# Optimization experiments

Measured on AMD Instinct MI355X. Metric: run time of the kernel, lower is better.

## Reference

```python
import jax, jax.numpy as jnp
import numpy as np


def _conv2d(x, w, b):
    # 3x3, stride 1, pad 1, NCHW
    y = jax.lax.conv_general_dilated(x, w, (1, 1), [(1, 1), (1, 1)],
                                     dimension_numbers=('NCHW', 'OIHW', 'NCHW'))
    return y + b[None, :, None, None]


def _bilinear(img, py, px):
    # img: [B,C,H,W]; py/px: [B,H,W] float sample coords; zero padding outside
    B, C, H, W = img.shape
    y0f = jnp.floor(py)
    x0f = jnp.floor(px)
    wy = (py - y0f)[:, None]  # [B,1,H,W]
    wx = (px - x0f)[:, None]
    y0 = y0f.astype(jnp.int32)
    x0 = x0f.astype(jnp.int32)
    flat = img.reshape(B, C, H * W)

    def g(iy, ix):
        valid = (iy >= 0) & (iy < H) & (ix >= 0) & (ix < W)
        idx = (jnp.clip(iy, 0, H - 1) * W + jnp.clip(ix, 0, W - 1)).reshape(B, 1, H * W)
        v = jnp.take_along_axis(flat, idx, axis=2).reshape(B, C, H, W)
        return v * valid[:, None].astype(img.dtype)

    return (g(y0, x0) * (1 - wy) * (1 - wx)
            + g(y0, x0 + 1) * (1 - wy) * wx
            + g(y0 + 1, x0) * wy * (1 - wx)
            + g(y0 + 1, x0 + 1) * wy * wx)


def _deform_conv(x, offset, w, b):
    # torchvision DeformConv2d v1: kernel 3, stride 1, pad 1, dil 1, no mask
    # offset: [B, 18, H, W]; channels (2k, 2k+1) = (dy, dx) for kernel tap k (row-major)
    B, C, H, W = x.shape
    gy = jnp.arange(H, dtype=x.dtype)[:, None]   # [H,1]
    gx = jnp.arange(W, dtype=x.dtype)[None, :]   # [1,W]
    acc = jnp.zeros((B, w.shape[0], H, W), x.dtype)
    for k in range(9):  # small fixed kernel loop keeps intermediates O(B*C*H*W)
        ky, kx = k // 3, k % 3
        py = gy + (ky - 1) + offset[:, 2 * k]
        px = gx + (kx - 1) + offset[:, 2 * k + 1]
        samp = _bilinear(x, py, px)                      # [B,C,H,W]
        acc = acc + jnp.einsum('bchw,oc->bohw', samp, w[:, :, ky, kx])
    return acc + b[None, :, None, None]


def setup_inputs() -> dict:
    key = jax.random.key(0)
    ks = jax.random.split(key, 4)
    B, C, H, W = 4, 64, 256, 256
    return {
        'content_feats': jax.random.normal(ks[0], (B, C, H, W), jnp.float32),
        'blur_feats': jax.random.normal(ks[1], (B, C, H, W), jnp.float32),
        'offset_w': jax.random.normal(ks[2], (27, C, 3, 3), jnp.float32) * 0.02,
        'offset_b': jnp.zeros((27,), jnp.float32),
        'dc_w': jax.random.normal(ks[3], (C, C, 3, 3), jnp.float32) * 0.05,
        'dc_b': jnp.zeros((C,), jnp.float32),
    }


def reference(content_feats, blur_feats, offset_w, offset_b, dc_w, dc_b):
    ow = _conv2d(blur_feats, offset_w, offset_b)   # [B,27,H,W]
    offset = ow[:, :18]                            # first 2*3*3 channels are offsets
    out = _deform_conv(content_feats, offset, dc_w, dc_b)
    return (out, offset)
```

## Files before the change

kernel.cpp:

```cpp
#include <hip/hip_runtime.h>

#define BB 4
#define CC 64
#define HH 256
#define WW 256
#define HWHW 65536

typedef __bf16 bf16x8 __attribute__((ext_vector_type(8)));
typedef float f32x16 __attribute__((ext_vector_type(16)));
typedef unsigned int uint2v __attribute__((ext_vector_type(2)));

__device__ __forceinline__ unsigned short f32_to_bf16(float s) {
    unsigned int xi = __builtin_bit_cast(unsigned int, s);
    unsigned int r = (xi + 0x7fffu + ((xi >> 16) & 1u)) >> 16;
    return (unsigned short)r;
}

__global__ void prep_weights(const float* __restrict__ offset_w,
                             const float* __restrict__ dc_w,
                             float* __restrict__ wA,
                             unsigned short* __restrict__ WB2) {
    int idx = blockIdx.x * 256 + threadIdx.x;
    const int NA = CC * 9 * 18;
    const int NB = 4 * 18 * 64 * 8;
    if (idx < NA) {
        int c = idx / (9 * 18);
        int k = (idx / 18) % 9;
        int o = idx % 18;
        wA[idx] = offset_w[(o * CC + c) * 9 + k];
    }
    int j = idx - NA;
    if (j >= 0 && j < NB) {
        int chunk = j / 9216;
        int rem = j - chunk * 9216;
        int kslot = rem >> 9;
        int n = (rem >> 3) & 63;
        int jj = rem & 7;
        int k_local = kslot * 8 + jj;
        int tap = k_local >> 4;
        int c_local = k_local & 15;
        int c = chunk * 16 + c_local;
        WB2[j] = f32_to_bf16(dc_w[(n * CC + c) * 9 + tap]);
    }
}

__global__ __launch_bounds__(256) void offset_conv(
    const float* __restrict__ blur, const float* __restrict__ wA,
    const float* __restrict__ ob, float* __restrict__ offout) {
    const int x = threadIdx.x;
    const int y = blockIdx.x & (HH - 1);
    const int b = blockIdx.x >> 8;

    int rb[3], cx[3];
    float m[9];
#pragma unroll
    for (int dy = 0; dy < 3; ++dy) {
        int yy = y + dy - 1;
        rb[dy] = min(max(yy, 0), HH - 1) * WW;
        bool vy = (yy >= 0) && (yy < HH);
#pragma unroll
        for (int dx = 0; dx < 3; ++dx) {
            int xx = x + dx - 1;
            bool v = vy && (xx >= 0) && (xx < WW);
            m[dy * 3 + dx] = v ? 1.0f : 0.0f;
        }
    }
#pragma unroll
    for (int dx = 0; dx < 3; ++dx) cx[dx] = min(max(x + dx - 1, 0), WW - 1);

    float acc[18];
#pragma unroll
    for (int o = 0; o < 18; ++o) acc[o] = ob[o];

    const float* img = blur + (size_t)b * CC * HWHW;
    for (int c = 0; c < CC; ++c) {
        const float* pl = img + c * HWHW;
        float s[9];
#pragma unroll
        for (int dy = 0; dy < 3; ++dy)
#pragma unroll
            for (int dx = 0; dx < 3; ++dx)
                s[dy * 3 + dx] = pl[rb[dy] + cx[dx]] * m[dy * 3 + dx];

        const float* wp = wA + c * 9 * 18;
#pragma unroll
        for (int k = 0; k < 9; ++k) {
            float sv = s[k];
#pragma unroll
            for (int o = 0; o < 18; ++o)
                acc[o] = fmaf(sv, wp[k * 18 + o], acc[o]);
        }
    }

    float* op = offout + ((size_t)b * 18) * HWHW + y * WW + x;
#pragma unroll
    for (int o = 0; o < 18; ++o) op[(size_t)o * HWHW] = acc[o];
}

__global__ __launch_bounds__(256) void nchw_to_nhwc(
    const float* __restrict__ in, float* __restrict__ ct) {
    __shared__ float tile[64][65];
    const int t = threadIdx.x;
    const int blk = blockIdx.x;
    const int xseg = blk & 3;
    const int y = (blk >> 2) & (HH - 1);
    const int b = blk >> 10;
    const int px = t & 63;
    const int q = t >> 6;

    const float* src = in + (size_t)b * CC * HWHW + y * WW + xseg * 64;
#pragma unroll
    for (int i = 0; i < 16; ++i) {
        const int c = i * 4 + q;
        tile[c][px] = src[(size_t)c * HWHW + px];
    }
    __syncthreads();
    float* dst = ct + ((size_t)b * HWHW + y * WW + xseg * 64) * 64;
#pragma unroll
    for (int i = 0; i < 16; ++i) {
        const int p = i * 4 + q;
        dst[(size_t)p * 64 + px] = tile[px][p];
    }
}

__global__ __launch_bounds__(256, 4) void deform_mfma_nhwc(
    const float* __restrict__ ct, const float* __restrict__ offs,
    const unsigned short* __restrict__ WB2, const float* __restrict__ bias,
    float* __restrict__ out) {
    __shared__ __align__(16) char ldsbuf[36864];
    unsigned int* sampU = (unsigned int*)ldsbuf;
    float4* stateW = (float4*)(ldsbuf + 18432);
    uint4* stateV = (uint4*)(ldsbuf + 27648);
    float* ldsOut = (float*)ldsbuf;

    const int t = threadIdx.x;
    const int blk = blockIdx.x;
    const int xseg = blk & 3;
    const int y = (blk >> 2) & (HH - 1);
    const int b = blk >> 10;

    {
        const float* offbase = offs + (size_t)b * 18 * HWHW + y * WW + xseg * 64;
        for (int i = t; i < 576; i += 256) {
            const int p = i & 63;
            const int tap = i >> 6;
            const int ky = tap / 3, kx = tap - ky * 3;
            const float offy = offbase[(size_t)(2 * tap) * HWHW + p];
            const float offx = offbase[(size_t)(2 * tap + 1) * HWHW + p];
            const float py = (float)(y + ky - 1) + offy;
            const float pxf = (float)(xseg * 64 + p + kx - 1) + offx;
            const float y0f = floorf(py), x0f = floorf(pxf);
            const float wy = py - y0f, wx = pxf - x0f;
            const int y0 = (int)y0f, x0 = (int)x0f;

            float a00 = (1.0f - wy) * (1.0f - wx);
            float a01 = (1.0f - wy) * wx;
            float a10 = wy * (1.0f - wx);
            float a11 = wy * wx;
            const bool vy0 = (y0 >= 0) && (y0 < HH);
            const bool vy1 = (y0 + 1 >= 0) && (y0 + 1 < HH);
            const bool vx0 = (x0 >= 0) && (x0 < WW);
            const bool vx1 = (x0 + 1 >= 0) && (x0 + 1 < WW);
            float4 w;
            w.x = (vy0 && vx0) ? a00 : 0.0f;
            w.y = (vy0 && vx1) ? a01 : 0.0f;
            w.z = (vy1 && vx0) ? a10 : 0.0f;
            w.w = (vy1 && vx1) ? a11 : 0.0f;

            const int y0c = min(max(y0, 0), HH - 1);
            const int y1c = min(max(y0 + 1, 0), HH - 1);
            const int x0c = min(max(x0, 0), WW - 1);
            const int x1c = min(max(x0 + 1, 0), WW - 1);
            const unsigned int v00 = (unsigned int)(y0c * WW + x0c) << 8;
            const unsigned int dxb = (unsigned int)(x1c - x0c) << 8;
            const unsigned int dyb = (unsigned int)(y1c - y0c) << 16;

            stateW[i] = w;
            uint4 v;
            v.x = v00;
            v.y = v00 + dxb;
            v.z = v00 + dyb;
            v.w = v00 + dyb + dxb;
            stateV[i] = v;
        }
    }
    __syncthreads();

    const char* ctb = (const char*)(ct + (size_t)b * HWHW * 64);

    f32x16 acc = {0, 0, 0, 0, 0, 0, 0, 0, 0, 0, 0, 0, 0, 0, 0, 0};

    const int lane = t & 63;
    const int wv = t >> 6;
    const int l3 = lane >> 3;
    const int clb = (lane & 7) * 8;
    const int hlf = lane >> 5;
    const int l31 = lane & 31;
    const int px_i = ((wv >> 1) * 32) + l31;
    const int n_i = ((wv & 1) * 32) + l31;

    for (int chunk = 0; chunk < 4; ++chunk) {
        {
            const int cb = chunk * 64 + clb;
#pragma unroll 6
            for (int it = 0; it < 18; ++it) {
                const int j = wv * 144 + it * 8 + l3;
                const float4 w = stateW[j];
                const uint4 vo = stateV[j];
                const float2 v00 = *(const float2*)(ctb + (vo.x + cb));
                const float2 v01 = *(const float2*)(ctb + (vo.y + cb));
                const float2 v10 = *(const float2*)(ctb + (vo.z + cb));
                const float2 v11 = *(const float2*)(ctb + (vo.w + cb));
                const float s0 = w.x * v00.x + w.y * v01.x + w.z * v10.x + w.w * v11.x;
                const float s1 = w.x * v00.y + w.y * v01.y + w.z * v10.y + w.w * v11.y;
                unsigned int pk;
                asm("v_cvt_pk_bf16_f32 %0, %1, %2" : "=v"(pk) : "v"(s0), "v"(s1));
                const int tap = j >> 6;
                const int px = j & 63;
                sampU[(tap * 2 + ((lane >> 2) & 1)) * 256 + px * 4 + (lane & 3)] = pk;
            }
        }
        __syncthreads();

        {
            const bf16x8* sampV = (const bf16x8*)sampU;
            const bf16x8* wV = (const bf16x8*)(WB2 + (size_t)chunk * 9216);
#pragma unroll
            for (int ks = 0; ks < 9; ++ks) {
                bf16x8 fa = sampV[(ks * 2 + hlf) * 64 + px_i];
                bf16x8 fb = wV[(ks * 2 + hlf) * 64 + n_i];
                acc = __builtin_amdgcn_mfma_f32_32x32x16_bf16(fa, fb, acc, 0, 0, 0);
            }
        }
        __syncthreads();
    }

    {
        const int n_l = (wv & 1) * 32 + l31;
        const int px_base = (wv >> 1) * 32 + 4 * hlf;
#pragma unroll
        for (int r = 0; r < 16; ++r) {
            const int row = px_base + (r & 3) + 8 * (r >> 2);
            ldsOut[n_l * 65 + row] = acc[r];
        }
    }
    __syncthreads();
    {
        float* base = out + (size_t)b * CC * HWHW + y * WW + xseg * 64;
        for (int i = t; i < 4096; i += 256) {
            const int n = i >> 6;
            const int p = i & 63;
            base[(size_t)n * HWHW + p] = ldsOut[n * 65 + p] + bias[n];
        }
    }
}

__global__ __launch_bounds__(256) void deform_mfma_gather(
    const float* __restrict__ content, const float* __restrict__ offs,
    const unsigned short* __restrict__ WB2, const float* __restrict__ bias,
    float* __restrict__ out) {
    __shared__ __align__(16) char ldsbuf[29952];
    unsigned int* sampU = (unsigned int*)ldsbuf;
    float4* stateW = (float4*)(ldsbuf + 18432);
    unsigned int* stateI = (unsigned int*)(ldsbuf + 27648);
    float* ldsOut = (float*)ldsbuf;

    const int t = threadIdx.x;
    const int px = t & 63;
    const int cg = t >> 6;
    const int blk = blockIdx.x;
    const int xseg = blk & 3;
    const int y = (blk >> 2) & (HH - 1);
    const int b = blk >> 10;

    {
        const float* offbase = offs + (size_t)b * 18 * HWHW + y * WW + xseg * 64;
        for (int i = t; i < 576; i += 256) {
            const int p = i & 63;
            const int tap = i >> 6;
            const int ky = tap / 3, kx = tap - ky * 3;
            const float offy = offbase[(size_t)(2 * tap) * HWHW + p];
            const float offx = offbase[(size_t)(2 * tap + 1) * HWHW + p];
            const float py = (float)(y + ky - 1) + offy;
            const float pxf = (float)(xseg * 64 + p + kx - 1) + offx;
            const float y0f = floorf(py), x0f = floorf(pxf);
            const float wy = py - y0f, wx = pxf - x0f;
            const int y0 = (int)y0f, x0 = (int)x0f;
            float a00 = (1.0f - wy) * (1.0f - wx);
            float a01 = (1.0f - wy) * wx;
            float a10 = wy * (1.0f - wx);
            float a11 = wy * wx;
            const bool vy0 = (y0 >= 0) && (y0 < HH);
            const bool vy1 = (y0 + 1 >= 0) && (y0 + 1 < HH);
            const bool vx0 = (x0 >= 0) && (x0 < WW);
            const bool vx1 = (x0 + 1 >= 0) && (x0 + 1 < WW);
            float4 w;
            w.x = (vy0 && vx0) ? a00 : 0.0f;
            w.y = (vy0 && vx1) ? a01 : 0.0f;
            w.z = (vy1 && vx0) ? a10 : 0.0f;
            w.w = (vy1 && vx1) ? a11 : 0.0f;
            const int y0c = min(max(y0, 0), HH - 1);
            const int y1c = min(max(y0 + 1, 0), HH - 1);
            const int x0c = min(max(x0, 0), WW - 1);
            const int x1c = min(max(x0 + 1, 0), WW - 1);
            stateW[i] = w;
            stateI[i] = (unsigned int)(y0c * WW + x0c) |
                        ((unsigned int)(x1c - x0c) << 16) |
                        ((unsigned int)(y1c - y0c) << 17);
        }
    }
    __syncthreads();

    const float* img = content + (size_t)b * CC * HWHW;
    f32x16 acc = {0, 0, 0, 0, 0, 0, 0, 0, 0, 0, 0, 0, 0, 0, 0, 0};
    const int lane = t & 63;
    const int hlf = lane >> 5;
    const int l31 = lane & 31;
    const int px_i = ((cg >> 1) * 32) + l31;
    const int n_i = ((cg & 1) * 32) + l31;

    for (int chunk = 0; chunk < 4; ++chunk) {
        const int cbase = (chunk * 16 + cg * 4) << 16;
#pragma unroll 3
        for (int tap = 0; tap < 9; ++tap) {
            const float4 w = stateW[tap * 64 + px];
            const unsigned int ii = stateI[tap * 64 + px];
            const int i0 = (int)(ii & 0xFFFFu);
            const int dx = (int)((ii >> 16) & 1u);
            const int dyw = ((int)((ii >> 17) & 1u)) << 8;
            unsigned int pk0 = 0, pk1 = 0;
#pragma unroll
            for (int i = 0; i < 4; ++i) {
                const int cb = cbase + (i << 16);
                const float v00 = img[cb + i0];
                const float v01 = img[cb + i0 + dx];
                const float v10 = img[cb + i0 + dyw];
                const float v11 = img[cb + i0 + dyw + dx];
                const float s = w.x * v00 + w.y * v01 + w.z * v10 + w.w * v11;
                const unsigned int u = f32_to_bf16(s);
                if (i == 0) pk0 = u;
                else if (i == 1) pk0 |= u << 16;
                else if (i == 2) pk1 = u;
                else pk1 |= u << 16;
            }
            uint2v v2 = {pk0, pk1};
            *(uint2v*)&sampU[(tap * 2 + (cg >> 1)) * 256 + px * 4 + (cg & 1) * 2] = v2;
        }
        __syncthreads();
        {
            const bf16x8* sampV = (const bf16x8*)sampU;
            const bf16x8* wV = (const bf16x8*)(WB2 + (size_t)chunk * 9216);
#pragma unroll
            for (int ks = 0; ks < 9; ++ks) {
                bf16x8 fa = sampV[(ks * 2 + hlf) * 64 + px_i];
                bf16x8 fb = wV[(ks * 2 + hlf) * 64 + n_i];
                acc = __builtin_amdgcn_mfma_f32_32x32x16_bf16(fa, fb, acc, 0, 0, 0);
            }
        }
        __syncthreads();
    }

    {
        const int n_l = (cg & 1) * 32 + l31;
        const int px_base = (cg >> 1) * 32 + 4 * hlf;
#pragma unroll
        for (int r = 0; r < 16; ++r) {
            const int row = px_base + (r & 3) + 8 * (r >> 2);
            ldsOut[n_l * 65 + row] = acc[r];
        }
    }
    __syncthreads();
    {
        float* base = out + (size_t)b * CC * HWHW + y * WW + xseg * 64;
        for (int i = t; i < 4096; i += 256) {
            const int n = i >> 6;
            const int p = i & 63;
            base[(size_t)n * HWHW + p] = ldsOut[n * 65 + p] + bias[n];
        }
    }
}

extern "C" void kernel_launch(void* const* d_in, const int* in_sizes, int n_in,
                              void* d_out, int out_size, void* d_ws, size_t ws_size,
                              hipStream_t stream) {
    const float* content  = (const float*)d_in[0];
    const float* blur     = (const float*)d_in[1];
    const float* offset_w = (const float*)d_in[2];
    const float* offset_b = (const float*)d_in[3];
    const float* dc_w     = (const float*)d_in[4];
    const float* dc_b     = (const float*)d_in[5];

    float* out0    = (float*)d_out;
    float* off_out = out0 + (size_t)BB * CC * HWHW;

    float* wA = (float*)d_ws;
    unsigned short* WB2 = (unsigned short*)(wA + CC * 9 * 18);

    const size_t CT_OFF = 131072;
    const size_t WS_NEED = CT_OFF + (size_t)BB * HWHW * CC * 4;

    const int NPREP = CC * 9 * 18 + 4 * 18 * 64 * 8;
    prep_weights<<<(NPREP + 255) / 256, 256, 0, stream>>>(offset_w, dc_w, wA, WB2);
    offset_conv<<<BB * HH, 256, 0, stream>>>(blur, wA, offset_b, off_out);

    if (ws_size >= WS_NEED) {
        float* ct = (float*)((char*)d_ws + CT_OFF);
        nchw_to_nhwc<<<BB * HH * 4, 256, 0, stream>>>(content, ct);
        deform_mfma_nhwc<<<BB * HH * 4, 256, 0, stream>>>(ct, off_out, WB2, dc_b, out0);
    } else {
        deform_mfma_gather<<<BB * HH * 4, 256, 0, stream>>>(content, off_out, WB2, dc_b, out0);
    }
}
```

Baseline: 433.5 us.

## Stage offset-conv rows via LDS, widen deform gathers, shrink sampling state

The offset conv now runs 512 threads per block. It stages three input rows for 16 channels into LDS with global_load_lds, splits the channels between two thread halves and reduces the partial sums through LDS. The deform kernel packs each tap's gather state into a single 32-bit word, which cuts LDS use enough to allow 5 blocks per CU. It also has each lane gather float4 (4 channels) instead of float2, halving loop iterations. s_setprio is raised around the MFMA loop. These changes aim to reduce redundant global loads and raise occupancy, at the cost of extra syncs and more register pressure.

```diff
diff --git a/kernel.cpp b/kernel.cpp
--- a/kernel.cpp
+++ b/kernel.cpp
@@ -9,6 +9,10 @@
 typedef __bf16 bf16x8 __attribute__((ext_vector_type(8)));
 typedef float f32x16 __attribute__((ext_vector_type(16)));
 typedef unsigned int uint2v __attribute__((ext_vector_type(2)));
+typedef unsigned int uint_t;
+
+typedef const unsigned int __attribute__((address_space(1))) gu32_t;
+typedef unsigned int __attribute__((address_space(3))) lu32_t;
 
 __device__ __forceinline__ unsigned short f32_to_bf16(float s) {
     unsigned int xi = __builtin_bit_cast(unsigned int, s);
@@ -44,10 +48,13 @@
     }
 }
 
-__global__ __launch_bounds__(256) void offset_conv(
+__global__ __launch_bounds__(512, 6) void offset_conv(
     const float* __restrict__ blur, const float* __restrict__ wA,
     const float* __restrict__ ob, float* __restrict__ offout) {
-    const int x = threadIdx.x;
+    __shared__ __align__(16) float rows[12288];
+    const int t = threadIdx.x;
+    const int x = t & 255;
+    const int h = t >> 8;
     const int y = blockIdx.x & (HH - 1);
     const int b = blockIdx.x >> 8;
 
@@ -70,31 +77,58 @@
 
     float acc[18];
 #pragma unroll
-    for (int o = 0; o < 18; ++o) acc[o] = ob[o];
-
-    const float* img = blur + (size_t)b * CC * HWHW;
-    for (int c = 0; c < CC; ++c) {
-        const float* pl = img + c * HWHW;
-        float s[9];
-#pragma unroll
-        for (int dy = 0; dy < 3; ++dy)
-#pragma unroll
-            for (int dx = 0; dx < 3; ++dx)
-                s[dy * 3 + dx] = pl[rb[dy] + cx[dx]] * m[dy * 3 + dx];
-
-        const float* wp = wA + c * 9 * 18;
-#pragma unroll
-        for (int k = 0; k < 9; ++k) {
-            float sv = s[k];
-#pragma unroll
-            for (int o = 0; o < 18; ++o)
-                acc[o] = fmaf(sv, wp[k * 18 + o], acc[o]);
-        }
-    }
-
-    float* op = offout + ((size_t)b * 18) * HWHW + y * WW + x;
-#pragma unroll
-    for (int o = 0; o < 18; ++o) op[(size_t)o * HWHW] = acc[o];
+    for (int o = 0; o < 18; ++o) acc[o] = (h == 0) ? ob[o] : 0.0f;
+
+    const float* blurb = blur + (size_t)b * CC * HWHW;
+    const int w8 = (t >> 6) * 256;
+
+    for (int chunk = 0; chunk < 4; ++chunk) {
+        const int c16 = chunk * 16;
+#pragma unroll
+        for (int s = 0; s < 6; ++s) {
+            const int f = s * 2048 + t * 4;
+            const int r = f >> 12;
+            const int c = (f >> 8) & 15;
+            const int col = f & 255;
+            const float* src = blurb + ((size_t)(c16 + c) << 16) + rb[r] + col;
+            __builtin_amdgcn_global_load_lds(
+                (gu32_t*)src, (lu32_t*)(rows + s * 2048 + w8), 16, 0, 0);
+        }
+        __syncthreads();
+
+#pragma unroll 2
+        for (int i = 0; i < 8; ++i) {
+            const int cc = h * 8 + i;
+            const float* base = rows + cc * 256;
+            float s9[9];
+#pragma unroll
+            for (int r = 0; r < 3; ++r)
+#pragma unroll
+                for (int dx = 0; dx < 3; ++dx)
+                    s9[r * 3 + dx] = base[r * 4096 + cx[dx]] * m[r * 3 + dx];
+            const float* wp = wA + (c16 + cc) * 162;
+#pragma unroll
+            for (int k = 0; k < 9; ++k) {
+                const float sv = s9[k];
+#pragma unroll
+                for (int o = 0; o < 18; ++o)
+                    acc[o] = fmaf(sv, wp[k * 18 + o], acc[o]);
+            }
+        }
+        __syncthreads();
+    }
+
+    if (h == 1) {
+#pragma unroll
+        for (int o = 0; o < 18; ++o) rows[o * 256 + x] = acc[o];
+    }
+    __syncthreads();
+    if (h == 0) {
+        float* op = offout + ((size_t)b * 18) * HWHW + y * WW + x;
+#pragma unroll
+        for (int o = 0; o < 18; ++o)
+            op[(size_t)o * HWHW] = acc[o] + rows[o * 256 + x];
+    }
 }
 
 __global__ __launch_bounds__(256) void nchw_to_nhwc(
@@ -123,14 +157,14 @@
     }
 }
 
-__global__ __launch_bounds__(256, 4) void deform_mfma_nhwc(
+__global__ __launch_bounds__(256, 5) void deform_mfma_nhwc(
     const float* __restrict__ ct, const float* __restrict__ offs,
     const unsigned short* __restrict__ WB2, const float* __restrict__ bias,
     float* __restrict__ out) {
-    __shared__ __align__(16) char ldsbuf[36864];
-    unsigned int* sampU = (unsigned int*)ldsbuf;
+    __shared__ __align__(16) char ldsbuf[29952];
+    uint_t* sampU = (uint_t*)ldsbuf;
     float4* stateW = (float4*)(ldsbuf + 18432);
-    uint4* stateV = (uint4*)(ldsbuf + 27648);
+    uint_t* stateC = (uint_t*)(ldsbuf + 27648);
     float* ldsOut = (float*)ldsbuf;
 
     const int t = threadIdx.x;
@@ -171,17 +205,11 @@
             const int y1c = min(max(y0 + 1, 0), HH - 1);
             const int x0c = min(max(x0, 0), WW - 1);
             const int x1c = min(max(x0 + 1, 0), WW - 1);
-            const unsigned int v00 = (unsigned int)(y0c * WW + x0c) << 8;
-            const unsigned int dxb = (unsigned int)(x1c - x0c) << 8;
-            const unsigned int dyb = (unsigned int)(y1c - y0c) << 16;
 
             stateW[i] = w;
-            uint4 v;
-            v.x = v00;
-            v.y = v00 + dxb;
-            v.z = v00 + dyb;
-            v.w = v00 + dyb + dxb;
-            stateV[i] = v;
+            stateC[i] = (uint_t)(y0c * WW + x0c) |
+                        ((uint_t)(x1c - x0c) << 16) |
+                        ((uint_t)(y1c - y0c) << 17);
         }
     }
     __syncthreads();
@@ -192,8 +220,10 @@
 
     const int lane = t & 63;
     const int wv = t >> 6;
-    const int l3 = lane >> 3;
-    const int clb = (lane & 7) * 8;
+    const int l4 = lane >> 2;
+    const int chq = lane & 3;
+    const int sS = chq >> 1;
+    const int sDw = (chq & 1) * 2;
     const int hlf = lane >> 5;
     const int l31 = lane & 31;
     const int px_i = ((wv >> 1) * 32) + l31;
@@ -201,23 +231,30 @@
 
     for (int chunk = 0; chunk < 4; ++chunk) {
         {
-            const int cb = chunk * 64 + clb;
-#pragma unroll 6
-            for (int it = 0; it < 18; ++it) {
-                const int j = wv * 144 + it * 8 + l3;
+            const int cb = chunk * 64 + chq * 16;
+#pragma unroll 3
+            for (int it = 0; it < 9; ++it) {
+                const int j = wv * 144 + it * 16 + l4;
                 const float4 w = stateW[j];
-                const uint4 vo = stateV[j];
-                const float2 v00 = *(const float2*)(ctb + (vo.x + cb));
-                const float2 v01 = *(const float2*)(ctb + (vo.y + cb));
-                const float2 v10 = *(const float2*)(ctb + (vo.z + cb));
-                const float2 v11 = *(const float2*)(ctb + (vo.w + cb));
+                const uint_t ii = stateC[j];
+                const uint_t a00 = (ii & 0xffffu) << 8;
+                const uint_t dxo = (ii & 0x10000u) >> 8;
+                const uint_t dyo = (ii & 0x20000u) >> 1;
+                const float4 v00 = *(const float4*)(ctb + (a00 + cb));
+                const float4 v01 = *(const float4*)(ctb + (a00 + dxo + cb));
+                const float4 v10 = *(const float4*)(ctb + (a00 + dyo + cb));
+                const float4 v11 = *(const float4*)(ctb + (a00 + dyo + dxo + cb));
                 const float s0 = w.x * v00.x + w.y * v01.x + w.z * v10.x + w.w * v11.x;
                 const float s1 = w.x * v00.y + w.y * v01.y + w.z * v10.y + w.w * v11.y;
-                unsigned int pk;
-                asm("v_cvt_pk_bf16_f32 %0, %1, %2" : "=v"(pk) : "v"(s0), "v"(s1));
+                const float s2 = w.x * v00.z + w.y * v01.z + w.z * v10.z + w.w * v11.z;
+                const float s3 = w.x * v00.w + w.y * v01.w + w.z * v10.w + w.w * v11.w;
+                uint_t pk0, pk1;
+                asm("v_cvt_pk_bf16_f32 %0, %1, %2" : "=v"(pk0) : "v"(s0), "v"(s1));
+                asm("v_cvt_pk_bf16_f32 %0, %1, %2" : "=v"(pk1) : "v"(s2), "v"(s3));
                 const int tap = j >> 6;
-                const int px = j & 63;
-                sampU[(tap * 2 + ((lane >> 2) & 1)) * 256 + px * 4 + (lane & 3)] = pk;
+                const int ppx = j & 63;
+                uint2v v2 = {pk0, pk1};
+                *(uint2v*)&sampU[(tap * 2 + sS) * 256 + ppx * 4 + sDw] = v2;
             }
         }
         __syncthreads();
@@ -225,12 +262,14 @@
         {
             const bf16x8* sampV = (const bf16x8*)sampU;
             const bf16x8* wV = (const bf16x8*)(WB2 + (size_t)chunk * 9216);
+            __builtin_amdgcn_s_setprio(1);
 #pragma unroll
             for (int ks = 0; ks < 9; ++ks) {
                 bf16x8 fa = sampV[(ks * 2 + hlf) * 64 + px_i];
                 bf16x8 fb = wV[(ks * 2 + hlf) * 64 + n_i];
                 acc = __builtin_amdgcn_mfma_f32_32x32x16_bf16(fa, fb, acc, 0, 0, 0);
             }
+            __builtin_amdgcn_s_setprio(0);
         }
         __syncthreads();
     }
@@ -260,9 +299,9 @@
     const unsigned short* __restrict__ WB2, const float* __restrict__ bias,
     float* __restrict__ out) {
     __shared__ __align__(16) char ldsbuf[29952];
-    unsigned int* sampU = (unsigned int*)ldsbuf;
+    uint_t* sampU = (uint_t*)ldsbuf;
     float4* stateW = (float4*)(ldsbuf + 18432);
-    unsigned int* stateI = (unsigned int*)(ldsbuf + 27648);
+    uint_t* stateI = (uint_t*)(ldsbuf + 27648);
     float* ldsOut = (float*)ldsbuf;
 
     const int t = threadIdx.x;
@@ -304,9 +343,9 @@
             const int x0c = min(max(x0, 0), WW - 1);
             const int x1c = min(max(x0 + 1, 0), WW - 1);
             stateW[i] = w;
-            stateI[i] = (unsigned int)(y0c * WW + x0c) |
-                        ((unsigned int)(x1c - x0c) << 16) |
-                        ((unsigned int)(y1c - y0c) << 17);
+            stateI[i] = (uint_t)(y0c * WW + x0c) |
+                        ((uint_t)(x1c - x0c) << 16) |
+                        ((uint_t)(y1c - y0c) << 17);
         }
     }
     __syncthreads();
@@ -324,11 +363,11 @@
 #pragma unroll 3
         for (int tap = 0; tap < 9; ++tap) {
             const float4 w = stateW[tap * 64 + px];
-            const unsigned int ii = stateI[tap * 64 + px];
+            const uint_t ii = stateI[tap * 64 + px];
             const int i0 = (int)(ii & 0xFFFFu);
             const int dx = (int)((ii >> 16) & 1u);
             const int dyw = ((int)((ii >> 17) & 1u)) << 8;
-            unsigned int pk0 = 0, pk1 = 0;
+            uint_t pk0 = 0, pk1 = 0;
 #pragma unroll
             for (int i = 0; i < 4; ++i) {
                 const int cb = cbase + (i << 16);
@@ -337,7 +376,7 @@
                 const float v10 = img[cb + i0 + dyw];
                 const float v11 = img[cb + i0 + dyw + dx];
                 const float s = w.x * v00 + w.y * v01 + w.z * v10 + w.w * v11;
-                const unsigned int u = f32_to_bf16(s);
+                const uint_t u = f32_to_bf16(s);
                 if (i == 0) pk0 = u;
                 else if (i == 1) pk0 |= u << 16;
                 else if (i == 2) pk1 = u;
@@ -401,7 +440,7 @@
 
     const int NPREP = CC * 9 * 18 + 4 * 18 * 64 * 8;
     prep_weights<<<(NPREP + 255) / 256, 256, 0, stream>>>(offset_w, dc_w, wA, WB2);
-    offset_conv<<<BB * HH, 256, 0, stream>>>(blur, wA, offset_b, off_out);
+    offset_conv<<<BB * HH, 512, 0, stream>>>(blur, wA, offset_b, off_out);
 
     if (ws_size >= WS_NEED) {
         float* ct = (float*)((char*)d_ws + CT_OFF);
```

New measurement: 821.6 us. +89.5%, slower.
